# Performance work log

Hardware: AMD Instinct MI355X
Metric: run time of the kernel (lower is better)

The kernel has to match this reference:

```python
import jax, jax.numpy as jnp
import numpy as np

T, B, D, H = 256, 64, 1024, 1024


def _linear_params(key, fan_in, shape_w, shape_b):
    kw, kb = jax.random.split(key)
    bound = 1.0 / np.sqrt(fan_in)
    W = jax.random.uniform(kw, shape_w, jnp.float32, -bound, bound)
    b = jax.random.uniform(kb, shape_b, jnp.float32, -bound, bound)
    return W, b


def setup_inputs() -> dict:
    key = jax.random.key(0)
    ks = jax.random.split(key, 6)
    x = jax.random.normal(ks[0], (T, B, D), jnp.float32)
    hidden = jnp.zeros((B, H), jnp.float32)
    cell = jnp.zeros((B, H), jnp.float32)
    W_in, b_in = _linear_params(ks[1], D, (H, D), (H,))
    W_hid, b_hid = _linear_params(ks[2], H, (H, H), (H,))
    # 4 gates (i, f, g, o), each with an x-path and h-path hidden->hidden Linear
    Wx_g, bx_g = _linear_params(ks[3], H, (4, H, H), (4, H))
    Wh_g, bh_g = _linear_params(ks[4], H, (4, H, H), (4, H))
    return {"x": x, "hidden": hidden, "cell": cell,
            "W_in": W_in, "b_in": b_in, "W_hid": W_hid, "b_hid": b_hid,
            "Wx_g": Wx_g, "bx_g": bx_g, "Wh_g": Wh_g, "bh_g": bh_g}


def reference(x, hidden, cell, W_in, b_in, W_hid, b_hid, Wx_g, bx_g, Wh_g, bh_g):
    # input_layer / hidden_layer projections, then 4 gate Linears per path,
    # mirroring the many-small-Linear LSTM cell of the torch module.
    def step(carry, x_t):
        h, c = carry
        x2h = x_t @ W_in.T + b_in          # [B, H]
        h2h = h @ W_hid.T + b_hid          # [B, H]
        g = (jnp.einsum('ghk,bk->gbh', Wx_g, x2h) + bx_g[:, None, :]
             + jnp.einsum('ghk,bk->gbh', Wh_g, h2h) + bh_g[:, None, :])  # [4, B, H]
        i = jax.nn.sigmoid(g[0])
        f = jax.nn.sigmoid(g[1])
        gg = jnp.tanh(g[2])
        o = jax.nn.sigmoid(g[3])
        c_new = f * c + i * gg
        h_new = o * jnp.tanh(c_new)
        return (h_new, c_new), None

    (h, c), _ = jax.lax.scan(step, (hidden, cell), x)
    return (h, c)
```

## Files before the change

### kernel.cpp

```cpp
#include <hip/hip_runtime.h>

typedef __attribute__((ext_vector_type(8))) short short8;
typedef __attribute__((ext_vector_type(4))) float f32x4;

#define SEQ_BLOCKS 64

__device__ __forceinline__ unsigned short f2bf(float f) {
  unsigned u = __float_as_uint(f);
  u = u + 0x7fffu + ((u >> 16) & 1u);
  return (unsigned short)(u >> 16);
}
__device__ __forceinline__ unsigned short f2h(float f) {
  _Float16 h = (_Float16)f;
  unsigned short r;
  __builtin_memcpy(&r, &h, 2);
  return r;
}
__device__ __forceinline__ float h2f(unsigned short u) {
  _Float16 h;
  __builtin_memcpy(&h, &u, 2);
  return (float)h;
}
__device__ __forceinline__ void gload16(const void* g, void* l) {
  __builtin_amdgcn_global_load_lds(
      (const __attribute__((address_space(1))) unsigned int*)g,
      (__attribute__((address_space(3))) unsigned int*)l, 16, 0, 0);
}
__device__ __forceinline__ float fast_sigmoid(float x) {
  return 1.0f / (1.0f + __expf(-x));
}
__device__ __forceinline__ float fast_tanh(float x) {
  return 2.0f / (1.0f + __expf(-2.0f * x)) - 1.0f;
}
__device__ __forceinline__ short8 load_h16(const unsigned short* p) {
  union { unsigned long long u[2]; short8 s; } r;
  r.u[0] = __hip_atomic_load((const unsigned long long*)p, __ATOMIC_RELAXED,
                             __HIP_MEMORY_SCOPE_AGENT);
  r.u[1] = __hip_atomic_load(((const unsigned long long*)p) + 1, __ATOMIC_RELAXED,
                             __HIP_MEMORY_SCOPE_AGENT);
  return r.s;
}

__global__ void k_conv_bf16(const float* __restrict__ in, unsigned short* __restrict__ out) {
  size_t i = ((size_t)blockIdx.x * 256 + threadIdx.x) * 4;
  float4 v = *(const float4*)(in + i);
  unsigned short o[4] = {f2bf(v.x), f2bf(v.y), f2bf(v.z), f2bf(v.w)};
  *(uint2*)(out + i) = *(const uint2*)o;
}

__global__ void k_h0t(const float* __restrict__ hidden, unsigned short* __restrict__ hT) {
  int sb = blockIdx.x;
  int row = threadIdx.x >> 2, c4 = (threadIdx.x & 3) * 4;
  float4 v = *(const float4*)(hidden + (size_t)row * 1024 + sb * 16 + c4);
  unsigned short o[4] = {f2bf(v.x), f2bf(v.y), f2bf(v.z), f2bf(v.w)};
  unsigned long long u;
  __builtin_memcpy(&u, o, 8);
  *(unsigned long long*)(hT + (size_t)sb * 1024 + row * 16 + c4) = u;
}

__global__ void k_transpose(const float* __restrict__ in, unsigned short* __restrict__ out,
                            int R, int C) {
  __shared__ float tile[32][33];
  int bx = blockIdx.x * 32, by = blockIdx.y * 32;
  int tx = threadIdx.x & 31, ty = threadIdx.x >> 5;
  for (int i = 0; i < 32; i += 8)
    tile[ty + i][tx] = in[(size_t)(by + ty + i) * C + bx + tx];
  __syncthreads();
  for (int i = 0; i < 32; i += 8)
    out[(size_t)(bx + ty + i) * R + by + tx] = f2bf(tile[tx][ty + i]);
}

template<int OUTMODE>
__global__ __launch_bounds__(256) void k_gemm_bt(
    const unsigned short* __restrict__ A, const unsigned short* __restrict__ B,
    unsigned short* __restrict__ C, const float* __restrict__ bias,
    int M, int N, int K) {
  __shared__ unsigned short As[128 * 32];
  __shared__ unsigned short Bs[128 * 32];
  const int tid = threadIdx.x;
  const int wv = tid >> 6, l = tid & 63;
  const int m0 = blockIdx.y * 128, n0 = blockIdx.x * 128;
  const int wr = (wv >> 1) * 64, wc = (wv & 1) * 64;
  f32x4 acc[4][4] = {};
  for (int k0 = 0; k0 < K; k0 += 32) {
#pragma unroll
    for (int j = 0; j < 2; ++j) {
      int c = wv * 128 + j * 64 + l;
      int row = c >> 2, kc = (c & 3) * 8;
      gload16(A + (size_t)(m0 + row) * K + k0 + kc, (char*)As + c * 16);
      gload16(B + (size_t)(n0 + row) * K + k0 + kc, (char*)Bs + c * 16);
    }
    __syncthreads();
    short8 af[4], bfr[4];
#pragma unroll
    for (int rf = 0; rf < 4; ++rf)
      af[rf] = *(const short8*)(As + (wr + rf * 16 + (l & 15)) * 32 + (l >> 4) * 8);
#pragma unroll
    for (int cf = 0; cf < 4; ++cf)
      bfr[cf] = *(const short8*)(Bs + (wc + cf * 16 + (l & 15)) * 32 + (l >> 4) * 8);
#pragma unroll
    for (int rf = 0; rf < 4; ++rf)
#pragma unroll
      for (int cf = 0; cf < 4; ++cf)
        acc[rf][cf] = __builtin_amdgcn_mfma_f32_16x16x32_bf16(af[rf], bfr[cf], acc[rf][cf], 0, 0, 0);
    __syncthreads();
  }
#pragma unroll
  for (int cf = 0; cf < 4; ++cf) {
    int col = n0 + wc + cf * 16 + (l & 15);
    float bv = bias ? bias[col] : 0.0f;
#pragma unroll
    for (int rf = 0; rf < 4; ++rf) {
#pragma unroll
      for (int i = 0; i < 4; ++i) {
        int row = m0 + wr + rf * 16 + (l >> 4) * 4 + i;
        float v = acc[rf][cf][i] + bv;
        if (OUTMODE == 0) {
          C[(size_t)row * N + col] = f2bf(v);
        } else {
          int t = row >> 6, b = row & 63;
          int g = col >> 10, c = col & 1023;
          size_t idx = (size_t)(t * 64 + (c >> 4)) * 4096 + (g * 64 + b) * 16 + (c & 15);
          C[idx] = f2h(v);
        }
      }
    }
  }
}

__global__ void k_bias(const float* __restrict__ Wxg, const float* __restrict__ bxg,
                       const float* __restrict__ b_in, const float* __restrict__ Whg,
                       const float* __restrict__ bhg, const float* __restrict__ b_hid,
                       float* __restrict__ gbias) {
  int col = blockIdx.x * 64 + (threadIdx.x >> 2);
  int p = threadIdx.x & 3;
  const float* wx = Wxg + (size_t)col * 1024;
  const float* wh = Whg + (size_t)col * 1024;
  float s = 0.f;
  for (int k = p * 256; k < p * 256 + 256; ++k)
    s += wx[k] * b_in[k] + wh[k] * b_hid[k];
  s += __shfl_down(s, 2, 4);
  s += __shfl_down(s, 1, 4);
  if (p == 0) gbias[col] = s + bxg[col] + bhg[col];
}

__global__ __launch_bounds__(256, 1) void k_lstm_seq(
    const unsigned short* __restrict__ GX2,
    const unsigned short* __restrict__ Whc,
    const float* __restrict__ cell,
    unsigned short* __restrict__ hT,
    float* __restrict__ out,
    unsigned* __restrict__ flags) {
  __shared__ float pbuf[64 * 261 + 4];
  const int tid = threadIdx.x;
  const int wv = tid >> 6, l = tid & 63;
  const int bid = blockIdx.x;

  short8 w[4][8];
#pragma unroll
  for (int ct = 0; ct < 4; ++ct)
#pragma unroll
    for (int u = 0; u < 8; ++u)
      w[ct][u] = *(const short8*)(
          Whc + (size_t)(ct * 1024 + bid * 16 + (l & 15)) * 1024 +
          wv * 256 + u * 32 + (l >> 4) * 8);

  const int eb = tid >> 2;
  const int ej = (tid & 3) * 4;
  float c_reg[4];
  {
    float4 c4 = *(const float4*)(cell + (size_t)eb * 1024 + bid * 16 + ej);
    c_reg[0] = c4.x; c_reg[1] = c4.y; c_reg[2] = c4.z; c_reg[3] = c4.w;
  }

  const size_t abase = (size_t)(wv * 16 + ((l >> 4) >> 1)) * 1024 + (l & 15) * 16 +
                       ((l >> 4) & 1) * 8;
  const unsigned* pollp = flags + (16 * wv + (l & 15)) * 64;

  for (int t = 0; t < 256; ++t) {
    const unsigned short* chunk = GX2 + ((size_t)t * 64 + bid) * 4096;
    unsigned long long gxu[4];
#pragma unroll
    for (int g = 0; g < 4; ++g)
      gxu[g] = *(const unsigned long long*)(chunk + (g * 64 + eb) * 16 + ej);

    if (t > 0) {
      const unsigned tgt = (unsigned)t;
      for (;;) {
        unsigned v = __hip_atomic_load(pollp, __ATOMIC_RELAXED, __HIP_MEMORY_SCOPE_AGENT);
        if (__all((int)(v >= tgt))) break;
        __builtin_amdgcn_s_sleep(1);
      }
      __builtin_amdgcn_fence(__ATOMIC_ACQUIRE, "workgroup");
    }

    const unsigned short* hb = hT + ((size_t)(t & 3) << 16) + abase;
    short8 a[4][8];
#pragma unroll
    for (int u = 0; u < 8; ++u)
#pragma unroll
      for (int rt = 0; rt < 4; ++rt)
        a[rt][u] = load_h16(hb + u * 2048 + rt * 256);

    f32x4 acc[4][4] = {};
#pragma unroll
    for (int u = 0; u < 8; ++u)
#pragma unroll
      for (int rt = 0; rt < 4; ++rt)
#pragma unroll
        for (int ct = 0; ct < 4; ++ct)
          acc[rt][ct] = __builtin_amdgcn_mfma_f32_16x16x32_bf16(a[rt][u], w[ct][u],
                                                                acc[rt][ct], 0, 0, 0);

#pragma unroll
    for (int rt = 0; rt < 4; ++rt)
#pragma unroll
      for (int ct = 0; ct < 4; ++ct)
#pragma unroll
        for (int i = 0; i < 4; ++i) {
          int b = rt * 16 + (l >> 4) * 4 + i;
          int gc = ct * 16 + (l & 15);
          int slot = (wv + gc + (b >> 2)) & 3;
          pbuf[b * 261 + gc * 4 + slot] = acc[rt][ct][i];
        }
    __syncthreads();

    float sgate[4][4];
#pragma unroll
    for (int g = 0; g < 4; ++g) {
      unsigned short gx4[4];
      __builtin_memcpy(gx4, &gxu[g], 8);
#pragma unroll
      for (int i2 = 0; i2 < 4; ++i2) {
        int gc = g * 16 + ej + i2;
        f32x4 p = *(const f32x4*)&pbuf[eb * 261 + gc * 4];
        sgate[g][i2] = p[0] + p[1] + p[2] + p[3] + h2f(gx4[i2]);
      }
    }
    float hnew[4];
#pragma unroll
    for (int i2 = 0; i2 < 4; ++i2) {
      float ig = fast_sigmoid(sgate[0][i2]);
      float fg = fast_sigmoid(sgate[1][i2]);
      float gg = fast_tanh(sgate[2][i2]);
      float og = fast_sigmoid(sgate[3][i2]);
      c_reg[i2] = fg * c_reg[i2] + ig * gg;
      hnew[i2] = og * fast_tanh(c_reg[i2]);
    }

    if (t == 255) {
      float4 h4 = {hnew[0], hnew[1], hnew[2], hnew[3]};
      float4 c4 = {c_reg[0], c_reg[1], c_reg[2], c_reg[3]};
      *(float4*)(out + (size_t)eb * 1024 + bid * 16 + ej) = h4;
      *(float4*)(out + 65536 + (size_t)eb * 1024 + bid * 16 + ej) = c4;
      __syncthreads();
    } else {
      unsigned short hs[4] = {f2bf(hnew[0]), f2bf(hnew[1]), f2bf(hnew[2]), f2bf(hnew[3])};
      unsigned long long hv;
      __builtin_memcpy(&hv, hs, 8);
      __hip_atomic_store(
          (unsigned long long*)(hT + ((size_t)((t + 1) & 3) << 16) + (size_t)bid * 1024 +
                                eb * 16 + ej),
          hv, __ATOMIC_RELAXED, __HIP_MEMORY_SCOPE_AGENT);
      asm volatile("s_waitcnt vmcnt(0)" ::: "memory");
      __syncthreads();
      if (tid == 0)
        __hip_atomic_store(&flags[bid * 64], (unsigned)(t + 1), __ATOMIC_RELAXED,
                           __HIP_MEMORY_SCOPE_AGENT);
    }
  }
}

extern "C" void kernel_launch(void* const* d_in, const int* in_sizes, int n_in,
                              void* d_out, int out_size, void* d_ws, size_t ws_size,
                              hipStream_t stream) {
  const float* x      = (const float*)d_in[0];
  const float* hidden = (const float*)d_in[1];
  const float* cell   = (const float*)d_in[2];
  const float* W_in   = (const float*)d_in[3];
  const float* b_in   = (const float*)d_in[4];
  const float* W_hid  = (const float*)d_in[5];
  const float* b_hid  = (const float*)d_in[6];
  const float* Wx_g   = (const float*)d_in[7];
  const float* bx_g   = (const float*)d_in[8];
  const float* Wh_g   = (const float*)d_in[9];
  const float* bh_g   = (const float*)d_in[10];
  float* out = (float*)d_out;

  char* ws = (char*)d_ws;
  unsigned short* GX2   = (unsigned short*)(ws);
  unsigned short* Xbf   = (unsigned short*)(ws + 134217728);
  unsigned short* WxGb  = (unsigned short*)(ws + 167772160);
  unsigned short* WhGb  = (unsigned short*)(ws + 176160768);
  unsigned short* WinT  = (unsigned short*)(ws + 184549376);
  unsigned short* WhidT = (unsigned short*)(ws + 186646528);
  unsigned short* Wxc   = (unsigned short*)(ws + 188743680);
  unsigned short* Whc   = (unsigned short*)(ws + 197132288);
  float*          gbias = (float*)(ws + 205520896);
  unsigned short* hT    = (unsigned short*)(ws + 134217728);
  unsigned*       flags = (unsigned*)(ws + 184549376);

  k_conv_bf16<<<16384, 256, 0, stream>>>(x, Xbf);
  k_conv_bf16<<<4096, 256, 0, stream>>>(Wx_g, WxGb);
  k_conv_bf16<<<4096, 256, 0, stream>>>(Wh_g, WhGb);
  k_transpose<<<dim3(32, 32), 256, 0, stream>>>(W_in, WinT, 1024, 1024);
  k_transpose<<<dim3(32, 32), 256, 0, stream>>>(W_hid, WhidT, 1024, 1024);
  k_gemm_bt<0><<<dim3(8, 32), 256, 0, stream>>>(WxGb, WinT, Wxc, nullptr, 4096, 1024, 1024);
  k_gemm_bt<0><<<dim3(8, 32), 256, 0, stream>>>(WhGb, WhidT, Whc, nullptr, 4096, 1024, 1024);
  k_bias<<<64, 256, 0, stream>>>(Wx_g, bx_g, b_in, Wh_g, bh_g, b_hid, gbias);
  k_gemm_bt<1><<<dim3(32, 128), 256, 0, stream>>>(Xbf, Wxc, GX2, gbias, 16384, 4096, 1024);
  k_h0t<<<64, 256, 0, stream>>>(hidden, hT);
  hipMemsetAsync(flags, 0, 64 * 64 * sizeof(unsigned), stream);
  k_lstm_seq<<<SEQ_BLOCKS, 256, 0, stream>>>(GX2, Whc, cell, hT, out, flags);
}
```

Measured before the change: 2.132 ms.

## Double-buffer LDS partials, vectorize partial stores, pack sync flags densely

The LDS partial-sum buffer is double-buffered by timestep parity, which allows dropping the trailing barrier on the last step. Each accumulator fragment is now stored as one f32x4 with an XOR swizzle instead of four scalar stores. Per-block flags are packed into a few contiguous cache lines instead of one flag per 256 bytes, so polling wavefronts touch fewer lines. The denser flags may add false sharing between writers, and the larger LDS footprint is only acceptable because one block runs per CU.

```diff
diff --git a/kernel.cpp b/kernel.cpp
--- a/kernel.cpp
+++ b/kernel.cpp
@@ -151,10 +151,11 @@
     unsigned short* __restrict__ hT,
     float* __restrict__ out,
     unsigned* __restrict__ flags) {
-  __shared__ float pbuf[64 * 261 + 4];
+  __shared__ float pbuf[34816];
   const int tid = threadIdx.x;
   const int wv = tid >> 6, l = tid & 63;
   const int bid = blockIdx.x;
+  const int a = l & 15, q = l >> 4;
 
   short8 w[4][8];
 #pragma unroll
@@ -162,8 +163,7 @@
 #pragma unroll
     for (int u = 0; u < 8; ++u)
       w[ct][u] = *(const short8*)(
-          Whc + (size_t)(ct * 1024 + bid * 16 + (l & 15)) * 1024 +
-          wv * 256 + u * 32 + (l >> 4) * 8);
+          Whc + (size_t)(ct * 1024 + bid * 16 + a) * 1024 + wv * 256 + u * 32 + q * 8);
 
   const int eb = tid >> 2;
   const int ej = (tid & 3) * 4;
@@ -173,9 +173,8 @@
     c_reg[0] = c4.x; c_reg[1] = c4.y; c_reg[2] = c4.z; c_reg[3] = c4.w;
   }
 
-  const size_t abase = (size_t)(wv * 16 + ((l >> 4) >> 1)) * 1024 + (l & 15) * 16 +
-                       ((l >> 4) & 1) * 8;
-  const unsigned* pollp = flags + (16 * wv + (l & 15)) * 64;
+  const size_t abase = (size_t)(wv * 16 + (q >> 1)) * 1024 + a * 16 + (q & 1) * 8;
+  const unsigned* pollp = flags + wv * 32 + a;
 
   for (int t = 0; t < 256; ++t) {
     const unsigned short* chunk = GX2 + ((size_t)t * 64 + bid) * 4096;
@@ -195,12 +194,12 @@
     }
 
     const unsigned short* hb = hT + ((size_t)(t & 3) << 16) + abase;
-    short8 a[4][8];
+    short8 afr[4][8];
 #pragma unroll
     for (int u = 0; u < 8; ++u)
 #pragma unroll
       for (int rt = 0; rt < 4; ++rt)
-        a[rt][u] = load_h16(hb + u * 2048 + rt * 256);
+        afr[rt][u] = load_h16(hb + u * 2048 + rt * 256);
 
     f32x4 acc[4][4] = {};
 #pragma unroll
@@ -209,43 +208,44 @@
       for (int rt = 0; rt < 4; ++rt)
 #pragma unroll
         for (int ct = 0; ct < 4; ++ct)
-          acc[rt][ct] = __builtin_amdgcn_mfma_f32_16x16x32_bf16(a[rt][u], w[ct][u],
+          acc[rt][ct] = __builtin_amdgcn_mfma_f32_16x16x32_bf16(afr[rt][u], w[ct][u],
                                                                 acc[rt][ct], 0, 0, 0);
 
+    const int pb = (t & 1) * 17408 + wv * 4352;
 #pragma unroll
     for (int rt = 0; rt < 4; ++rt)
 #pragma unroll
-      for (int ct = 0; ct < 4; ++ct)
-#pragma unroll
-        for (int i = 0; i < 4; ++i) {
-          int b = rt * 16 + (l >> 4) * 4 + i;
-          int gc = ct * 16 + (l & 15);
-          int slot = (wv + gc + (b >> 2)) & 3;
-          pbuf[b * 261 + gc * 4 + slot] = acc[rt][ct][i];
-        }
+      for (int ct = 0; ct < 4; ++ct) {
+        int gc = a * 4 + ct;
+        int b0 = (rt * 16 + q * 4) ^ ((((gc) >> 3) & 3) << 2);
+        *(f32x4*)&pbuf[pb + gc * 68 + b0] = acc[rt][ct];
+      }
     __syncthreads();
 
-    float sgate[4][4];
+    const int pr = (t & 1) * 17408;
+    float sg[4][4];
 #pragma unroll
     for (int g = 0; g < 4; ++g) {
       unsigned short gx4[4];
       __builtin_memcpy(gx4, &gxu[g], 8);
 #pragma unroll
-      for (int i2 = 0; i2 < 4; ++i2) {
-        int gc = g * 16 + ej + i2;
-        f32x4 p = *(const f32x4*)&pbuf[eb * 261 + gc * 4];
-        sgate[g][i2] = p[0] + p[1] + p[2] + p[3] + h2f(gx4[i2]);
+      for (int i = 0; i < 4; ++i) {
+        int gc = (ej + i) * 4 + g;
+        int bx = eb ^ ((((gc) >> 3) & 3) << 2);
+        float s = pbuf[pr + 0 * 4352 + gc * 68 + bx] + pbuf[pr + 1 * 4352 + gc * 68 + bx] +
+                  pbuf[pr + 2 * 4352 + gc * 68 + bx] + pbuf[pr + 3 * 4352 + gc * 68 + bx];
+        sg[g][i] = s + h2f(gx4[i]);
       }
     }
     float hnew[4];
 #pragma unroll
-    for (int i2 = 0; i2 < 4; ++i2) {
-      float ig = fast_sigmoid(sgate[0][i2]);
-      float fg = fast_sigmoid(sgate[1][i2]);
-      float gg = fast_tanh(sgate[2][i2]);
-      float og = fast_sigmoid(sgate[3][i2]);
-      c_reg[i2] = fg * c_reg[i2] + ig * gg;
-      hnew[i2] = og * fast_tanh(c_reg[i2]);
+    for (int i = 0; i < 4; ++i) {
+      float ig = fast_sigmoid(sg[0][i]);
+      float fg = fast_sigmoid(sg[1][i]);
+      float gg = fast_tanh(sg[2][i]);
+      float og = fast_sigmoid(sg[3][i]);
+      c_reg[i] = fg * c_reg[i] + ig * gg;
+      hnew[i] = og * fast_tanh(c_reg[i]);
     }
 
     if (t == 255) {
@@ -253,7 +253,6 @@
       float4 c4 = {c_reg[0], c_reg[1], c_reg[2], c_reg[3]};
       *(float4*)(out + (size_t)eb * 1024 + bid * 16 + ej) = h4;
       *(float4*)(out + 65536 + (size_t)eb * 1024 + bid * 16 + ej) = c4;
-      __syncthreads();
     } else {
       unsigned short hs[4] = {f2bf(hnew[0]), f2bf(hnew[1]), f2bf(hnew[2]), f2bf(hnew[3])};
       unsigned long long hv;
@@ -265,8 +264,8 @@
       asm volatile("s_waitcnt vmcnt(0)" ::: "memory");
       __syncthreads();
       if (tid == 0)
-        __hip_atomic_store(&flags[bid * 64], (unsigned)(t + 1), __ATOMIC_RELAXED,
-                           __HIP_MEMORY_SCOPE_AGENT);
+        __hip_atomic_store(&flags[(bid >> 4) * 32 + (bid & 15)], (unsigned)(t + 1),
+                           __ATOMIC_RELAXED, __HIP_MEMORY_SCOPE_AGENT);
     }
   }
 }
@@ -310,6 +309,6 @@
   k_bias<<<64, 256, 0, stream>>>(Wx_g, bx_g, b_in, Wh_g, bh_g, b_hid, gbias);
   k_gemm_bt<1><<<dim3(32, 128), 256, 0, stream>>>(Xbf, Wxc, GX2, gbias, 16384, 4096, 1024);
   k_h0t<<<64, 256, 0, stream>>>(hidden, hT);
-  hipMemsetAsync(flags, 0, 64 * 64 * sizeof(unsigned), stream);
+  hipMemsetAsync(flags, 0, 512, stream);
   k_lstm_seq<<<SEQ_BLOCKS, 256, 0, stream>>>(GX2, Whc, cell, hT, out, flags);
 }
```

New measurement: 2.206 ms. 1.03x slower.
